# Performance work log

Hardware: AMD Instinct MI355X
Metric: run time of the kernel (lower is better)

Reference implementation:

```python
import jax, jax.numpy as jnp
import numpy as np

V, D, H, L, FF, T, B, W = 32000, 1024, 16, 8, 4096, 1024, 2, 256
HALF = FF // 2
HD = D // H
EPS = 1e-5


def layer_norm(x, g, b):
    mu = jnp.mean(x, axis=-1, keepdims=True)
    var = jnp.mean(jnp.square(x - mu), axis=-1, keepdims=True)
    return (x - mu) * jax.lax.rsqrt(var + EPS) * g + b


def setup_inputs() -> dict:
    key = jax.random.key(0)
    ks = jax.random.split(key, 12)
    s = 0.02
    nrm = lambda k, shape: jax.random.normal(k, shape, jnp.float32) * s
    idx = jax.random.randint(ks[0], (B, T), 0, V, dtype=jnp.int64)
    return {
        "idx": idx,
        "tok_emb": nrm(ks[1], (V, D)),
        "pos_emb": nrm(ks[2], (T, D)),
        "ln1_g": jnp.ones((L, D), jnp.float32),
        "ln1_b": jnp.zeros((L, D), jnp.float32),
        "qkv_w": nrm(ks[3], (L, 3 * D, D)),
        "out_w": nrm(ks[4], (L, D, D)),
        "ln2_g": jnp.ones((L, D), jnp.float32),
        "ln2_b": jnp.zeros((L, D), jnp.float32),
        "a_w1": nrm(ks[5], (L, HALF, D)),
        "a_w2": nrm(ks[6], (L, D, HALF)),
        "f_w1": nrm(ks[7], (L, HALF, D)),
        "f_w2": nrm(ks[8], (L, D, HALF)),
        "lnf_g": jnp.ones((D,), jnp.float32),
        "lnf_b": jnp.zeros((D,), jnp.float32),
        "head_w": nrm(ks[9], (V, D)),
    }


def _forward(idx, tok_emb, pos_emb, ln1_g, ln1_b, qkv_w, out_w, ln2_g, ln2_b,
             a_w1, a_w2, f_w1, f_w2, lnf_g, lnf_b, head_w):
    Bc, Tc = idx.shape
    x = tok_emb[idx] + pos_emb[:Tc]  # [B,T,D]
    # sliding-window causal band: attend to j in [i-W+1, i]
    i = jnp.arange(Tc)
    d = i[:, None] - i[None, :]
    mask = jnp.where((d >= 0) & (d < W), 0.0, -jnp.inf).astype(x.dtype)  # [T,T]
    scale = 1.0 / np.sqrt(HD)

    def block(x, p):
        l1g, l1b, qw, ow, l2g, l2b, aw1, aw2, fw1, fw2 = p
        h = layer_norm(x, l1g, l1b)
        qkv = (h @ qw.T).reshape(Bc, Tc, 3, H, HD)
        q, k, v = qkv[:, :, 0], qkv[:, :, 1], qkv[:, :, 2]  # [B,T,H,HD]
        attn = jnp.einsum('bqhd,bkhd->bhqk', q, k) * scale + mask
        attn = jax.nn.softmax(attn, axis=-1)
        o = jnp.einsum('bhqk,bkhd->bqhd', attn, v).reshape(Bc, Tc, D)
        x = x + o @ ow.T
        h2 = layer_norm(x, l2g, l2b)
        mlp = (jax.nn.gelu(h2 @ aw1.T, approximate=False) @ aw2.T
               + jax.nn.gelu(h2 @ fw1.T, approximate=False) @ fw2.T)
        return x + mlp, None

    x, _ = jax.lax.scan(block, x, (ln1_g, ln1_b, qkv_w, out_w, ln2_g, ln2_b,
                                   a_w1, a_w2, f_w1, f_w2))
    return layer_norm(x, lnf_g, lnf_b) @ head_w.T  # [B,T,V]


def reference(idx, tok_emb, pos_emb, ln1_g, ln1_b, qkv_w, out_w, ln2_g, ln2_b,
              a_w1, a_w2, f_w1, f_w2, lnf_g, lnf_b, head_w):
    return _forward(idx, tok_emb, pos_emb, ln1_g, ln1_b, qkv_w, out_w,
                    ln2_g, ln2_b, a_w1, a_w2, f_w1, f_w2, lnf_g, lnf_b, head_w)
```

## Files before the change

kernel.cpp:

```cpp
#include <hip/hip_runtime.h>

typedef __bf16 bf16x8 __attribute__((ext_vector_type(8)));
typedef __bf16 bf16x4 __attribute__((ext_vector_type(4)));
typedef float  f32x4  __attribute__((ext_vector_type(4)));
typedef unsigned int u32x4 __attribute__((ext_vector_type(4)));

#define MFMA16(a, b, c) __builtin_amdgcn_mfma_f32_16x16x32_bf16(a, b, c, 0, 0, 0)

__device__ __forceinline__ void gload_lds16(const void* g, void* l) {
  __builtin_amdgcn_global_load_lds(
      (const __attribute__((address_space(1))) void*)g,
      (__attribute__((address_space(3))) void*)l, 16, 0, 0);
}

__device__ __forceinline__ void waitvm(int vm) {
  if (vm == 10)     asm volatile("s_waitcnt vmcnt(10)" ::: "memory");
  else if (vm == 8) asm volatile("s_waitcnt vmcnt(8)" ::: "memory");
  else if (vm == 6) asm volatile("s_waitcnt vmcnt(6)" ::: "memory");
  else if (vm == 4) asm volatile("s_waitcnt vmcnt(4)" ::: "memory");
  else if (vm == 3) asm volatile("s_waitcnt vmcnt(3)" ::: "memory");
  else              asm volatile("s_waitcnt vmcnt(0)" ::: "memory");
}

__global__ __launch_bounds__(256) void cvt_kernel(
    const float* __restrict__ s, __bf16* __restrict__ d, int n8) {
  int i = blockIdx.x * 256 + threadIdx.x;
  if (i >= n8) return;
  size_t o = (size_t)i * 8;
  f32x4 a = *(const f32x4*)(s + o), b = *(const f32x4*)(s + o + 4);
  bf16x8 v;
  v[0] = (__bf16)a[0]; v[1] = (__bf16)a[1]; v[2] = (__bf16)a[2]; v[3] = (__bf16)a[3];
  v[4] = (__bf16)b[0]; v[5] = (__bf16)b[1]; v[6] = (__bf16)b[2]; v[7] = (__bf16)b[3];
  *(bf16x8*)(d + o) = v;
}

__global__ __launch_bounds__(256) void cat_w1_kernel(
    const float* __restrict__ a, const float* __restrict__ f, __bf16* __restrict__ d) {
  int i = blockIdx.x * 256 + threadIdx.x;
  int k = (i & 127) * 8;
  int r = i >> 7;
  const float* s = (r < 2048) ? a + ((size_t)r << 10) + k
                              : f + ((size_t)(r - 2048) << 10) + k;
  f32x4 va = *(const f32x4*)s, vb = *(const f32x4*)(s + 4);
  bf16x8 v;
  v[0] = (__bf16)va[0]; v[1] = (__bf16)va[1]; v[2] = (__bf16)va[2]; v[3] = (__bf16)va[3];
  v[4] = (__bf16)vb[0]; v[5] = (__bf16)vb[1]; v[6] = (__bf16)vb[2]; v[7] = (__bf16)vb[3];
  *(bf16x8*)(d + ((size_t)i << 3)) = v;
}

__global__ __launch_bounds__(256) void cat_w2_kernel(
    const float* __restrict__ a, const float* __restrict__ f, __bf16* __restrict__ d) {
  int i = blockIdx.x * 256 + threadIdx.x;
  int k = (i & 511) * 8;
  int r = i >> 9;
  const float* s = (k < 2048) ? a + (size_t)r * 2048 + k
                              : f + (size_t)r * 2048 + (k - 2048);
  f32x4 va = *(const f32x4*)s, vb = *(const f32x4*)(s + 4);
  bf16x8 v;
  v[0] = (__bf16)va[0]; v[1] = (__bf16)va[1]; v[2] = (__bf16)va[2]; v[3] = (__bf16)va[3];
  v[4] = (__bf16)vb[0]; v[5] = (__bf16)vb[1]; v[6] = (__bf16)vb[2]; v[7] = (__bf16)vb[3];
  *(bf16x8*)(d + ((size_t)i << 3)) = v;
}

__global__ __launch_bounds__(256) void embed_kernel(
    const int* __restrict__ idx, const float* __restrict__ te,
    const float* __restrict__ pe, float* __restrict__ x) {
  int m = blockIdx.x;
  int t = m & 1023;
  int tok = idx[m];
  int c = threadIdx.x * 4;
  f32x4 a = *(const f32x4*)(te + (size_t)tok * 1024 + c);
  f32x4 p = *(const f32x4*)(pe + (size_t)t * 1024 + c);
  *(f32x4*)(x + (size_t)m * 1024 + c) = a + p;
}

__global__ __launch_bounds__(256) void ln_kernel(
    const float* __restrict__ x, const float* __restrict__ g,
    const float* __restrict__ bb, __bf16* __restrict__ out) {
  int row = blockIdx.x, tid = threadIdx.x;
  int wid = tid >> 6, lane = tid & 63;
  f32x4 v = *(const f32x4*)(x + (size_t)row * 1024 + tid * 4);
  float s = v[0] + v[1] + v[2] + v[3];
  #pragma unroll
  for (int off = 32; off >= 1; off >>= 1) s += __shfl_xor(s, off);
  __shared__ float red1[4], red2[4];
  if (lane == 0) red1[wid] = s;
  __syncthreads();
  float mu = (red1[0] + red1[1] + red1[2] + red1[3]) * (1.0f / 1024.0f);
  float d0 = v[0] - mu, d1 = v[1] - mu, d2 = v[2] - mu, d3 = v[3] - mu;
  float q = d0 * d0 + d1 * d1 + d2 * d2 + d3 * d3;
  #pragma unroll
  for (int off = 32; off >= 1; off >>= 1) q += __shfl_xor(q, off);
  if (lane == 0) red2[wid] = q;
  __syncthreads();
  float var = (red2[0] + red2[1] + red2[2] + red2[3]) * (1.0f / 1024.0f);
  float inv = rsqrtf(var + 1e-5f);
  f32x4 gg = *(const f32x4*)(g + tid * 4);
  f32x4 bv = *(const f32x4*)(bb + tid * 4);
  bf16x4 o4;
  o4[0] = (__bf16)(d0 * inv * gg[0] + bv[0]);
  o4[1] = (__bf16)(d1 * inv * gg[1] + bv[1]);
  o4[2] = (__bf16)(d2 * inv * gg[2] + bv[2]);
  o4[3] = (__bf16)(d3 * inv * gg[3] + bv[3]);
  *(bf16x4*)(out + (size_t)row * 1024 + tid * 4) = o4;
}

template <int EPI>
__global__ __launch_bounds__(512, 1) void gemm256(
    const __bf16* __restrict__ A, int lda,
    const __bf16* __restrict__ B, int ldb, int K,
    float* __restrict__ Cf, __bf16* __restrict__ Cb, int ldc, int nbx) {
  __shared__ __align__(16) __bf16 lds[65536];
  const int tid = threadIdx.x, lane = tid & 63, w = tid >> 6;
  const int l15 = lane & 15, l4 = lane >> 4;
  const int wr = w >> 2, wc = w & 3;

  int nwg = gridDim.x, id = blockIdx.x;
  int q = nwg >> 3, r = nwg & 7;
  int xcd = id & 7, pos = id >> 3;
  int nid = (xcd < r ? xcd * (q + 1) : r * (q + 1) + (xcd - r) * q) + pos;
  int row0 = (nid % nbx) * 256, col0 = (nid / nbx) * 256;

  const __bf16* ag = A + (size_t)row0 * lda;
  const __bf16* bg = B + (size_t)col0 * ldb;

  f32x4 acc[8][4];
  #pragma unroll
  for (int i = 0; i < 8; ++i)
    #pragma unroll
    for (int j = 0; j < 4; ++j) acc[i][j] = (f32x4){0.f, 0.f, 0.f, 0.f};

  int srow[2], scol[2];
  #pragma unroll
  for (int i = 0; i < 2; ++i) {
    int p = (w + i * 8) * 1024 + lane * 16;
    int row = p >> 6, ch = (p >> 4) & 3;
    srow[i] = row;
    scol[i] = (ch ^ ((row >> 1) & 3)) * 8;
  }
  const int fx = (((l4 << 4) ^ (((l15 >> 1) & 3) << 4)) >> 1);

  auto stageA = [&](int t, int c) {
    #pragma unroll
    for (int i = 0; i < 2; ++i)
      gload_lds16(ag + (size_t)srow[i] * lda + t * 32 + scol[i],
                  &lds[c * 16384 + (w + i * 8) * 512]);
  };
  auto stageB = [&](int t, int c) {
    #pragma unroll
    for (int i = 0; i < 2; ++i)
      gload_lds16(bg + (size_t)srow[i] * ldb + t * 32 + scol[i],
                  &lds[c * 16384 + 8192 + (w + i * 8) * 512]);
  };

  auto kgroup = [&](int t2, int c, int cn, int vm, bool stg) {
    if (stg) stageA(t2, cn);
    waitvm(vm);
    __builtin_amdgcn_sched_barrier(0);
    __builtin_amdgcn_s_barrier();
    __builtin_amdgcn_sched_barrier(0);
    const int cb = c * 16384;
    bf16x8 bfr[4], af[4];
    #pragma unroll
    for (int ni = 0; ni < 4; ++ni)
      bfr[ni] = *(const bf16x8*)&lds[cb + 8192 + (wc * 64 + ni * 16 + l15) * 32 + fx];
    #pragma unroll
    for (int mi = 0; mi < 4; ++mi)
      af[mi] = *(const bf16x8*)&lds[cb + (wr * 128 + mi * 16 + l15) * 32 + fx];
    __builtin_amdgcn_s_setprio(1);
    #pragma unroll
    for (int mi = 0; mi < 4; ++mi)
      #pragma unroll
      for (int ni = 0; ni < 4; ++ni)
        acc[mi][ni] = MFMA16(af[mi], bfr[ni], acc[mi][ni]);
    __builtin_amdgcn_s_setprio(0);
    #pragma unroll
    for (int mi = 0; mi < 4; ++mi)
      af[mi] = *(const bf16x8*)&lds[cb + (wr * 128 + (mi + 4) * 16 + l15) * 32 + fx];
    if (stg) stageB(t2, cn);
    __builtin_amdgcn_s_setprio(1);
    #pragma unroll
    for (int mi = 0; mi < 4; ++mi)
      #pragma unroll
      for (int ni = 0; ni < 4; ++ni)
        acc[mi + 4][ni] = MFMA16(af[mi], bfr[ni], acc[mi + 4][ni]);
    __builtin_amdgcn_s_setprio(0);
    __builtin_amdgcn_sched_barrier(0);
    __builtin_amdgcn_s_barrier();
    __builtin_amdgcn_sched_barrier(0);
  };

  const int NT = K >> 5;
  stageA(0, 0); stageB(0, 0);
  stageA(1, 1); stageB(1, 1);
  stageA(2, 2); stageB(2, 2);

  int c = 0;
  for (int t = 0; t < NT - 3; ++t) {
    int cn = c + 3; if (cn >= 4) cn -= 4;
    kgroup(t + 3, c, cn, 10, true);
    c = (c + 1) & 3;
  }
  kgroup(0, c, 0, 8, false); c = (c + 1) & 3;
  kgroup(0, c, 0, 4, false); c = (c + 1) & 3;
  kgroup(0, c, 0, 0, false);

  #pragma unroll
  for (int mi = 0; mi < 8; ++mi)
    #pragma unroll
    for (int ni = 0; ni < 4; ++ni)
      #pragma unroll
      for (int rr = 0; rr < 4; ++rr) {
        int row = row0 + wr * 128 + mi * 16 + l4 * 4 + rr;
        int col = col0 + wc * 64 + ni * 16 + l15;
        float v = acc[mi][ni][rr];
        size_t off = (size_t)row * ldc + col;
        if (EPI == 0) {
          Cf[off] = v;
        } else if (EPI == 1) {
          Cb[off] = (__bf16)v;
        } else {
          float gv = 0.5f * v * (1.0f + erff(v * 0.70710678118654752f));
          Cb[off] = (__bf16)gv;
        }
      }
}

template <int BN, int EPI>
__global__ __launch_bounds__(256) void gemm_bf16(
    const __bf16* __restrict__ A, int lda,
    const __bf16* __restrict__ B, int ldb, int K,
    float* __restrict__ Cf, __bf16* __restrict__ Cb, int ldc,
    const float* __restrict__ resid, int nbx) {
  constexpr int ACCN = BN / 32;
  constexpr int LB = BN / 64;
  constexpr int L = 2 + LB;
  __shared__ __align__(16) __bf16 As[3 * 4096];
  __shared__ __align__(16) __bf16 Bs[3 * BN * 32];

  int nwg = gridDim.x, id = blockIdx.x;
  int q = nwg >> 3, r = nwg & 7;
  int xcd = id & 7, pos = id >> 3;
  int nid = (xcd < r ? xcd * (q + 1) : r * (q + 1) + (xcd - r) * q) + pos;
  int row0 = (nid % nbx) * 128;
  int col0 = (nid / nbx) * BN;

  const int tid = threadIdx.x, lane = tid & 63, wid = tid >> 6;
  const int l15 = lane & 15, l4 = lane >> 4;
  const int wr = wid >> 1, wc = wid & 1;
  const int fx = (((l4 << 4) ^ (((l15 >> 1) & 3) << 4)) >> 1);

  f32x4 acc[4][ACCN];
  #pragma unroll
  for (int i = 0; i < 4; ++i)
    #pragma unroll
    for (int j = 0; j < ACCN; ++j) acc[i][j] = (f32x4){0.f, 0.f, 0.f, 0.f};

  const __bf16* aptr = A + (size_t)row0 * lda;
  const __bf16* bptr = B + (size_t)col0 * ldb;

  auto stage = [&](int t, int p) {
    #pragma unroll
    for (int i = 0; i < 2; ++i) {
      int ch = tid + 256 * i;
      int rr = ch >> 2, kc = ch & 3;
      gload_lds16(aptr + (size_t)rr * lda + t * 32 + (kc ^ ((rr >> 1) & 3)) * 8,
                  &As[p * 4096 + ch * 8]);
    }
    #pragma unroll
    for (int i = 0; i < LB; ++i) {
      int ch = tid + 256 * i;
      int rr = ch >> 2, kc = ch & 3;
      gload_lds16(bptr + (size_t)rr * ldb + t * 32 + (kc ^ ((rr >> 1) & 3)) * 8,
                  &Bs[p * BN * 32 + ch * 8]);
    }
  };

  const int NT = K >> 5;
  stage(0, 0);
  stage(1, 1);
  int p = 0;
  for (int t = 0; t < NT; ++t) {
    bool stg = (t + 2 < NT);
    if (stg) {
      int ps = p + 2; if (ps >= 3) ps -= 3;
      stage(t + 2, ps);
    }
    waitvm(stg ? 2 * L : ((t + 1 < NT) ? L : 0));
    __builtin_amdgcn_sched_barrier(0);
    __builtin_amdgcn_s_barrier();
    __builtin_amdgcn_sched_barrier(0);
    bf16x8 af[4], bfr[ACCN];
    #pragma unroll
    for (int mi = 0; mi < 4; ++mi)
      af[mi] = *(const bf16x8*)&As[p * 4096 + (wr * 64 + mi * 16 + l15) * 32 + fx];
    #pragma unroll
    for (int ni = 0; ni < ACCN; ++ni)
      bfr[ni] = *(const bf16x8*)&Bs[p * BN * 32 + (wc * (BN / 2) + ni * 16 + l15) * 32 + fx];
    __builtin_amdgcn_s_setprio(1);
    #pragma unroll
    for (int mi = 0; mi < 4; ++mi)
      #pragma unroll
      for (int ni = 0; ni < ACCN; ++ni)
        acc[mi][ni] = MFMA16(af[mi], bfr[ni], acc[mi][ni]);
    __builtin_amdgcn_s_setprio(0);
    __builtin_amdgcn_sched_barrier(0);
    __builtin_amdgcn_s_barrier();
    __builtin_amdgcn_sched_barrier(0);
    p = (p == 2) ? 0 : p + 1;
  }

  #pragma unroll
  for (int mi = 0; mi < 4; ++mi)
    #pragma unroll
    for (int ni = 0; ni < ACCN; ++ni)
      #pragma unroll
      for (int rr = 0; rr < 4; ++rr) {
        int row = row0 + wr * 64 + mi * 16 + l4 * 4 + rr;
        int col = col0 + wc * (BN / 2) + ni * 16 + l15;
        float v = acc[mi][ni][rr];
        size_t off = (size_t)row * ldc + col;
        if (EPI == 0) {
          Cf[off] = v;
        } else if (EPI == 1) {
          Cb[off] = (__bf16)v;
        } else if (EPI == 2) {
          float gv = 0.5f * v * (1.0f + erff(v * 0.70710678118654752f));
          Cb[off] = (__bf16)gv;
        } else {
          Cf[off] = resid[off] + v;
        }
      }
}

__global__ __launch_bounds__(256) void attn_kernel(
    const __bf16* __restrict__ qkv, __bf16* __restrict__ o) {
  const int bid = blockIdx.x;
  const int qt = bid & 15, h = (bid >> 4) & 15, b = bid >> 8;
  const int qs = qt * 64;
  const int ntiles = (qt + 1 < 5) ? (qt + 1) : 5;
  const int kt0 = qt - (ntiles - 1);

  __shared__ __align__(16) __bf16 Qs[64][72];
  __shared__ __align__(16) __bf16 KVs[64][72];
  __shared__ __align__(16) __bf16 Ssm[64][328];
  __shared__ float rsum[64];

  const int tid = threadIdx.x;
  const int lane = tid & 63, wid = tid >> 6;
  const int l15 = lane & 15, l4 = lane >> 4;
  const size_t rs = 3072;
  const __bf16* qbase = qkv + ((size_t)(b * 1024 + qs)) * rs + h * 64;

  #pragma unroll
  for (int i = 0; i < 2; ++i) {
    int c = tid * 2 + i;
    int rr = c >> 3, dc = c & 7;
    *(u32x4*)&Qs[rr][dc * 8] = *(const u32x4*)(qbase + (size_t)rr * rs + dc * 8);
  }

  for (int it = 0; it < ntiles; ++it) {
    int kt = kt0 + it;
    const __bf16* kbase = qkv + ((size_t)(b * 1024 + kt * 64)) * rs + 1024 + h * 64;
    __syncthreads();
    #pragma unroll
    for (int i = 0; i < 2; ++i) {
      int c = tid * 2 + i;
      int rr = c >> 3, dc = c & 7;
      *(u32x4*)&KVs[rr][dc * 8] = *(const u32x4*)(kbase + (size_t)rr * rs + dc * 8);
    }
    __syncthreads();
    bf16x8 aq[2];
    #pragma unroll
    for (int kk = 0; kk < 2; ++kk)
      aq[kk] = *(const bf16x8*)&Qs[16 * wid + l15][kk * 32 + l4 * 8];
    #pragma unroll
    for (int n = 0; n < 4; ++n) {
      f32x4 c4 = (f32x4){0.f, 0.f, 0.f, 0.f};
      #pragma unroll
      for (int kk = 0; kk < 2; ++kk) {
        bf16x8 bk = *(const bf16x8*)&KVs[n * 16 + l15][kk * 32 + l4 * 8];
        c4 = MFMA16(aq[kk], bk, c4);
      }
      int kj = kt * 64 + n * 16 + l15;
      int colS = it * 64 + n * 16 + l15;
      #pragma unroll
      for (int rr = 0; rr < 4; ++rr) {
        int qi = qs + 16 * wid + l4 * 4 + rr;
        int d = qi - kj;
        float sv = c4[rr] * 0.125f;
        Ssm[16 * wid + l4 * 4 + rr][colS] =
            (d >= 0 && d < 256) ? (__bf16)sv : (__bf16)(-1e30f);
      }
    }
  }

  for (int rr = 0; rr < 16; ++rr) {
    int row = 16 * wid + rr;
    float vals[5];
    #pragma unroll
    for (int i = 0; i < 5; ++i) vals[i] = -3e38f;
    #pragma unroll
    for (int i = 0; i < 5; ++i)
      if (i < ntiles) vals[i] = (float)Ssm[row][lane + 64 * i];
    float m = vals[0];
    #pragma unroll
    for (int i = 1; i < 5; ++i) m = fmaxf(m, vals[i]);
    #pragma unroll
    for (int off = 32; off >= 1; off >>= 1) m = fmaxf(m, __shfl_xor(m, off));
    float s = 0.f;
    #pragma unroll
    for (int i = 0; i < 5; ++i)
      if (i < ntiles) {
        float pp = __expf(vals[i] - m);
        s += pp;
        Ssm[row][lane + 64 * i] = (__bf16)pp;
      }
    #pragma unroll
    for (int off = 32; off >= 1; off >>= 1) s += __shfl_xor(s, off);
    if (lane == 0) rsum[row] = s;
  }

  f32x4 oacc[4];
  #pragma unroll
  for (int n = 0; n < 4; ++n) oacc[n] = (f32x4){0.f, 0.f, 0.f, 0.f};

  for (int it = 0; it < ntiles; ++it) {
    int kt = kt0 + it;
    const __bf16* vbase = qkv + ((size_t)(b * 1024 + kt * 64)) * rs + 2048 + h * 64;
    __syncthreads();
    {
      int k0 = (tid >> 4) * 4, d0 = (tid & 15) * 4;
      bf16x4 vr[4];
      #pragma unroll
      for (int rr = 0; rr < 4; ++rr)
        vr[rr] = *(const bf16x4*)(vbase + (size_t)(k0 + rr) * rs + d0);
      #pragma unroll
      for (int j = 0; j < 4; ++j) {
        bf16x4 wv;
        #pragma unroll
        for (int rr = 0; rr < 4; ++rr) wv[rr] = vr[rr][j];
        *(bf16x4*)&KVs[d0 + j][k0] = wv;
      }
    }
    __syncthreads();
    #pragma unroll
    for (int kk = 0; kk < 2; ++kk) {
      bf16x8 ap = *(const bf16x8*)&Ssm[16 * wid + l15][it * 64 + kk * 32 + l4 * 8];
      #pragma unroll
      for (int n = 0; n < 4; ++n) {
        bf16x8 bv = *(const bf16x8*)&KVs[n * 16 + l15][kk * 32 + l4 * 8];
        oacc[n] = MFMA16(ap, bv, oacc[n]);
      }
    }
  }

  #pragma unroll
  for (int n = 0; n < 4; ++n)
    #pragma unroll
    for (int rr = 0; rr < 4; ++rr) {
      int qrow = 16 * wid + l4 * 4 + rr;
      float inv = 1.0f / rsum[qrow];
      size_t m = (size_t)(b * 1024 + qs + qrow);
      o[m * 1024 + h * 64 + n * 16 + l15] = (__bf16)(oacc[n][rr] * inv);
    }
}

extern "C" void kernel_launch(void* const* d_in, const int* in_sizes, int n_in,
                              void* d_out, int out_size, void* d_ws, size_t ws_size,
                              hipStream_t stream) {
  (void)in_sizes; (void)n_in; (void)out_size;
  const int*   idx     = (const int*)d_in[0];
  const float* tok_emb = (const float*)d_in[1];
  const float* pos_emb = (const float*)d_in[2];
  const float* ln1_g   = (const float*)d_in[3];
  const float* ln1_b   = (const float*)d_in[4];
  const float* qkv_w   = (const float*)d_in[5];
  const float* out_w   = (const float*)d_in[6];
  const float* ln2_g   = (const float*)d_in[7];
  const float* ln2_b   = (const float*)d_in[8];
  const float* a_w1    = (const float*)d_in[9];
  const float* a_w2    = (const float*)d_in[10];
  const float* f_w1    = (const float*)d_in[11];
  const float* f_w2    = (const float*)d_in[12];
  const float* lnf_g   = (const float*)d_in[13];
  const float* lnf_b   = (const float*)d_in[14];
  const float* head_w  = (const float*)d_in[15];
  float* out = (float*)d_out;

  char* ws = (char*)d_ws;
  float*  x    = (float*)(ws);
  __bf16* h    = (__bf16*)(ws + 8388608);
  __bf16* qkv  = (__bf16*)(ws + 12582912);
  __bf16* oatt = (__bf16*)(ws + 25165824);
  __bf16* gcat = (__bf16*)(ws + 29360128);

  const bool full = ws_size >= 313000000ull;

  __bf16 *wq, *wo, *w1c, *w2c, *wh;
  if (full) {
    wq  = (__bf16*)(ws + 46137344);
    wo  = (__bf16*)(ws + 96468992);
    w1c = (__bf16*)(ws + 113246208);
    w2c = (__bf16*)(ws + 180355072);
    wh  = (__bf16*)(ws + 247463936);
    cvt_kernel<<<12288, 256, 0, stream>>>(qkv_w, wq, 3145728);
    cvt_kernel<<<4096, 256, 0, stream>>>(out_w, wo, 1048576);
    for (int l = 0; l < 8; ++l) {
      cat_w1_kernel<<<2048, 256, 0, stream>>>(
          a_w1 + (size_t)l * 2048 * 1024, f_w1 + (size_t)l * 2048 * 1024,
          w1c + (size_t)l * 4096 * 1024);
      cat_w2_kernel<<<2048, 256, 0, stream>>>(
          a_w2 + (size_t)l * 1024 * 2048, f_w2 + (size_t)l * 1024 * 2048,
          w2c + (size_t)l * 1024 * 4096);
    }
    cvt_kernel<<<16000, 256, 0, stream>>>(head_w, wh, 4096000);
  } else {
    wq  = (__bf16*)(ws + 46137344);
    wo  = (__bf16*)(ws + 52428800);
    w1c = (__bf16*)(ws + 54525952);
    w2c = (__bf16*)(ws + 62914560);
    wh  = (__bf16*)(ws + 46137344);
  }

  embed_kernel<<<2048, 256, 0, stream>>>(idx, tok_emb, pos_emb, x);

  for (int l = 0; l < 8; ++l) {
    const __bf16 *wq_l, *wo_l, *w1_l, *w2_l;
    if (full) {
      wq_l = wq + (size_t)l * 3072 * 1024;
      wo_l = wo + (size_t)l * 1024 * 1024;
      w1_l = w1c + (size_t)l * 4096 * 1024;
      w2_l = w2c + (size_t)l * 1024 * 4096;
    } else {
      cvt_kernel<<<1536, 256, 0, stream>>>(qkv_w + (size_t)l * 3072 * 1024, wq, 393216);
      cvt_kernel<<<512, 256, 0, stream>>>(out_w + (size_t)l * 1024 * 1024, wo, 131072);
      cat_w1_kernel<<<2048, 256, 0, stream>>>(
          a_w1 + (size_t)l * 2048 * 1024, f_w1 + (size_t)l * 2048 * 1024, w1c);
      cat_w2_kernel<<<2048, 256, 0, stream>>>(
          a_w2 + (size_t)l * 1024 * 2048, f_w2 + (size_t)l * 1024 * 2048, w2c);
      wq_l = wq; wo_l = wo; w1_l = w1c; w2_l = w2c;
    }

    ln_kernel<<<2048, 256, 0, stream>>>(x, ln1_g + l * 1024, ln1_b + l * 1024, h);
    gemm_bf16<128, 1><<<16 * 24, 256, 0, stream>>>(
        h, 1024, wq_l, 1024, 1024, nullptr, qkv, 3072, nullptr, 16);
    attn_kernel<<<512, 256, 0, stream>>>(qkv, oatt);
    gemm_bf16<64, 3><<<16 * 16, 256, 0, stream>>>(
        oatt, 1024, wo_l, 1024, 1024, x, nullptr, 1024, x, 16);
    ln_kernel<<<2048, 256, 0, stream>>>(x, ln2_g + l * 1024, ln2_b + l * 1024, h);
    gemm_bf16<128, 2><<<16 * 32, 256, 0, stream>>>(
        h, 1024, w1_l, 1024, 1024, nullptr, gcat, 4096, nullptr, 16);
    gemm_bf16<64, 3><<<16 * 16, 256, 0, stream>>>(
        gcat, 4096, w2_l, 4096, 4096, x, nullptr, 1024, x, 16);
  }

  if (!full) {
    cvt_kernel<<<16000, 256, 0, stream>>>(head_w, wh, 4096000);
  }
  ln_kernel<<<2048, 256, 0, stream>>>(x, lnf_g, lnf_b, h);
  gemm256<0><<<8 * 125, 512, 0, stream>>>(
      h, 1024, wh, 1024, 1024, out, nullptr, 32000, 8);
}
```

Before: 1.983 ms.

## Shrink GEMM pipeline to double buffer, batch weight-concat launches, retile softmax rows

```diff
diff --git a/kernel.cpp b/kernel.cpp
--- a/kernel.cpp
+++ b/kernel.cpp
@@ -19,6 +19,7 @@
   else if (vm == 6) asm volatile("s_waitcnt vmcnt(6)" ::: "memory");
   else if (vm == 4) asm volatile("s_waitcnt vmcnt(4)" ::: "memory");
   else if (vm == 3) asm volatile("s_waitcnt vmcnt(3)" ::: "memory");
+  else if (vm == 2) asm volatile("s_waitcnt vmcnt(2)" ::: "memory");
   else              asm volatile("s_waitcnt vmcnt(0)" ::: "memory");
 }
 
@@ -32,6 +33,38 @@
   v[0] = (__bf16)a[0]; v[1] = (__bf16)a[1]; v[2] = (__bf16)a[2]; v[3] = (__bf16)a[3];
   v[4] = (__bf16)b[0]; v[5] = (__bf16)b[1]; v[6] = (__bf16)b[2]; v[7] = (__bf16)b[3];
   *(bf16x8*)(d + o) = v;
+}
+
+__global__ __launch_bounds__(256) void cat_w1_all(
+    const float* __restrict__ a, const float* __restrict__ f, __bf16* __restrict__ d) {
+  int i = blockIdx.x * 256 + threadIdx.x;
+  int l = i >> 19, il = i & 524287;
+  int k = (il & 127) * 8;
+  int r = il >> 7;
+  const float* s = (r < 2048)
+      ? a + (size_t)l * 2097152 + ((size_t)r << 10) + k
+      : f + (size_t)l * 2097152 + ((size_t)(r - 2048) << 10) + k;
+  f32x4 va = *(const f32x4*)s, vb = *(const f32x4*)(s + 4);
+  bf16x8 v;
+  v[0] = (__bf16)va[0]; v[1] = (__bf16)va[1]; v[2] = (__bf16)va[2]; v[3] = (__bf16)va[3];
+  v[4] = (__bf16)vb[0]; v[5] = (__bf16)vb[1]; v[6] = (__bf16)vb[2]; v[7] = (__bf16)vb[3];
+  *(bf16x8*)(d + ((size_t)i << 3)) = v;
+}
+
+__global__ __launch_bounds__(256) void cat_w2_all(
+    const float* __restrict__ a, const float* __restrict__ f, __bf16* __restrict__ d) {
+  int i = blockIdx.x * 256 + threadIdx.x;
+  int l = i >> 19, il = i & 524287;
+  int k = (il & 511) * 8;
+  int r = il >> 9;
+  const float* s = (k < 2048)
+      ? a + (size_t)l * 2097152 + (size_t)r * 2048 + k
+      : f + (size_t)l * 2097152 + (size_t)r * 2048 + (k - 2048);
+  f32x4 va = *(const f32x4*)s, vb = *(const f32x4*)(s + 4);
+  bf16x8 v;
+  v[0] = (__bf16)va[0]; v[1] = (__bf16)va[1]; v[2] = (__bf16)va[2]; v[3] = (__bf16)va[3];
+  v[4] = (__bf16)vb[0]; v[5] = (__bf16)vb[1]; v[6] = (__bf16)vb[2]; v[7] = (__bf16)vb[3];
+  *(bf16x8*)(d + ((size_t)i << 3)) = v;
 }
 
 __global__ __launch_bounds__(256) void cat_w1_kernel(
@@ -106,11 +139,11 @@
 }
 
 template <int EPI>
-__global__ __launch_bounds__(512, 1) void gemm256(
+__global__ __launch_bounds__(512, 4) void gemm256(
     const __bf16* __restrict__ A, int lda,
     const __bf16* __restrict__ B, int ldb, int K,
     float* __restrict__ Cf, __bf16* __restrict__ Cb, int ldc, int nbx) {
-  __shared__ __align__(16) __bf16 lds[65536];
+  __shared__ __align__(16) __bf16 lds[32768];
   const int tid = threadIdx.x, lane = tid & 63, w = tid >> 6;
   const int l15 = lane & 15, l4 = lane >> 4;
   const int wr = w >> 2, wc = w & 3;
@@ -192,18 +225,10 @@
 
   const int NT = K >> 5;
   stageA(0, 0); stageB(0, 0);
-  stageA(1, 1); stageB(1, 1);
-  stageA(2, 2); stageB(2, 2);
-
-  int c = 0;
-  for (int t = 0; t < NT - 3; ++t) {
-    int cn = c + 3; if (cn >= 4) cn -= 4;
-    kgroup(t + 3, c, cn, 10, true);
-    c = (c + 1) & 3;
-  }
-  kgroup(0, c, 0, 8, false); c = (c + 1) & 3;
-  kgroup(0, c, 0, 4, false); c = (c + 1) & 3;
-  kgroup(0, c, 0, 0, false);
+  for (int t = 0; t < NT; ++t) {
+    const bool stg = (t + 1 < NT);
+    kgroup(t + 1, t & 1, (t + 1) & 1, stg ? 2 : 0, stg);
+  }
 
   #pragma unroll
   for (int mi = 0; mi < 8; ++mi)
@@ -394,31 +419,33 @@
       }
     }
   }
-
-  for (int rr = 0; rr < 16; ++rr) {
-    int row = 16 * wid + rr;
-    float vals[5];
-    #pragma unroll
-    for (int i = 0; i < 5; ++i) vals[i] = -3e38f;
-    #pragma unroll
-    for (int i = 0; i < 5; ++i)
-      if (i < ntiles) vals[i] = (float)Ssm[row][lane + 64 * i];
+  __syncthreads();
+
+  const int nc = ntiles * 4;
+  for (int ro = 0; ro < 4; ++ro) {
+    int row = 16 * wid + ro * 4 + l4;
+    float vals[20];
+    #pragma unroll
+    for (int i = 0; i < 20; ++i) vals[i] = -3e38f;
+    #pragma unroll
+    for (int i = 0; i < 20; ++i)
+      if (i < nc) vals[i] = (float)Ssm[row][l15 + 16 * i];
     float m = vals[0];
     #pragma unroll
-    for (int i = 1; i < 5; ++i) m = fmaxf(m, vals[i]);
-    #pragma unroll
-    for (int off = 32; off >= 1; off >>= 1) m = fmaxf(m, __shfl_xor(m, off));
+    for (int i = 1; i < 20; ++i) m = fmaxf(m, vals[i]);
+    #pragma unroll
+    for (int off = 8; off >= 1; off >>= 1) m = fmaxf(m, __shfl_xor(m, off));
     float s = 0.f;
     #pragma unroll
-    for (int i = 0; i < 5; ++i)
-      if (i < ntiles) {
+    for (int i = 0; i < 20; ++i)
+      if (i < nc) {
         float pp = __expf(vals[i] - m);
         s += pp;
-        Ssm[row][lane + 64 * i] = (__bf16)pp;
-      }
-    #pragma unroll
-    for (int off = 32; off >= 1; off >>= 1) s += __shfl_xor(s, off);
-    if (lane == 0) rsum[row] = s;
+        Ssm[row][l15 + 16 * i] = (__bf16)pp;
+      }
+    #pragma unroll
+    for (int off = 8; off >= 1; off >>= 1) s += __shfl_xor(s, off);
+    if (l15 == 0) rsum[row] = s;
   }
 
   f32x4 oacc[4];
@@ -506,14 +533,8 @@
     wh  = (__bf16*)(ws + 247463936);
     cvt_kernel<<<12288, 256, 0, stream>>>(qkv_w, wq, 3145728);
     cvt_kernel<<<4096, 256, 0, stream>>>(out_w, wo, 1048576);
-    for (int l = 0; l < 8; ++l) {
-      cat_w1_kernel<<<2048, 256, 0, stream>>>(
-          a_w1 + (size_t)l * 2048 * 1024, f_w1 + (size_t)l * 2048 * 1024,
-          w1c + (size_t)l * 4096 * 1024);
-      cat_w2_kernel<<<2048, 256, 0, stream>>>(
-          a_w2 + (size_t)l * 1024 * 2048, f_w2 + (size_t)l * 1024 * 2048,
-          w2c + (size_t)l * 1024 * 4096);
-    }
+    cat_w1_all<<<16384, 256, 0, stream>>>(a_w1, f_w1, w1c);
+    cat_w2_all<<<16384, 256, 0, stream>>>(a_w2, f_w2, w2c);
     cvt_kernel<<<16000, 256, 0, stream>>>(head_w, wh, 4096000);
   } else {
     wq  = (__bf16*)(ws + 46137344);
```

Result: slower. 2.985 ms (+50.6%).
